# Optimization experiments

Measured on AMD Instinct MI355X. Metric: run time of the kernel, lower is better.

Reference implementation:

```python
import jax, jax.numpy as jnp
import numpy as np

NUM_HEADS = 8
ALPHA = 4.0
BN_EPS = 1e-5


def _dwconv(x, w, pad):
    # x: [B, C, H, W], w: [C, 1, kh, kw] depthwise (groups == C)
    return jax.lax.conv_general_dilated(
        x, w, window_strides=(1, 1), padding=[(pad, pad), (pad, pad)],
        dimension_numbers=('NCHW', 'OIHW', 'NCHW'),
        feature_group_count=x.shape[1])


def _forward(x, qg_w, kv_w, proj_w, proj_b, dwc_w, dwc_b, power_p, scale_p,
             enh_w, bn_gamma, bn_beta, enhance_weight, pos_enc):
    B, N, C = x.shape
    H = W = int(round(N ** 0.5))
    h = NUM_HEADS
    d = C // h

    # qg linear (no bias): [B, N, 2C] -> q, g
    qg = jnp.einsum('bnc,oc->bno', x, qg_w)
    q, g = qg[..., :C], qg[..., C:]

    # SpatialFilterEnhancer on q: depthwise 3x3 conv + BN(train) + ReLU
    qi = q.transpose(0, 2, 1).reshape(B, C, H, W)
    qe = _dwconv(qi, enh_w, pad=1)
    m = qe.mean(axis=(0, 2, 3), keepdims=True)
    var = qe.var(axis=(0, 2, 3), keepdims=True)
    qe = (qe - m) * jax.lax.rsqrt(var + BN_EPS)
    qe = qe * bn_gamma[None, :, None, None] + bn_beta[None, :, None, None]
    qe = jax.nn.relu(qe)
    q_enh = qe.reshape(B, C, N).transpose(0, 2, 1)
    q = q + enhance_weight * q_enh

    # kv linear (sr_ratio == 1 path)
    kv = jnp.einsum('bnc,oc->bno', x, kv_w)
    k, v = kv[..., :C], kv[..., C:]
    k = k + pos_enc  # learned positional encoding, shape [1, N, C]
    n = k.shape[1]

    scale = jax.nn.softplus(scale_p)              # [1, 1, C]
    power = 1.0 + ALPHA * jax.nn.sigmoid(power_p)  # [1, h, 1, d]
    q = q / scale
    k = k / scale

    # split heads: [B, h, N, d]
    q = q.reshape(B, N, h, d).transpose(0, 2, 1, 3)
    k = k.reshape(B, n, h, d).transpose(0, 2, 1, 3)
    v = v.reshape(B, n, h, d).transpose(0, 2, 1, 3)

    # power-law kernel feature maps
    q_pos = jax.nn.relu(q) ** power
    q_neg = jax.nn.relu(-q) ** power
    k_pos = jax.nn.relu(k) ** power
    k_neg = jax.nn.relu(-k) ** power
    q_sim = jnp.concatenate([q_pos, q_neg], axis=-1)   # [B, h, N, 2d]
    q_opp = jnp.concatenate([q_neg, q_pos], axis=-1)
    kf = jnp.concatenate([k_pos, k_neg], axis=-1)      # [B, h, n, 2d]
    v1, v2 = jnp.split(v, 2, axis=-1)                  # [B, h, n, d/2] each

    k_mean = kf.mean(axis=-2)  # [B, h, 2d]
    inv_n = 1.0 / n

    # sim branch
    z = 1.0 / (jnp.einsum('bhnd,bhd->bhn', q_sim, k_mean)[..., None] + 1e-6)
    kv1 = jnp.einsum('bhnd,bhne->bhde', kf, v1) * inv_n  # (n^-0.5)*(n^-0.5)
    x_sim = jnp.einsum('bhnd,bhde->bhne', q_sim, kv1) * z

    # opp branch
    z2 = 1.0 / (jnp.einsum('bhnd,bhd->bhn', q_opp, k_mean)[..., None] + 1e-6)
    kv2 = jnp.einsum('bhnd,bhne->bhde', kf, v2) * inv_n
    x_opp = jnp.einsum('bhnd,bhde->bhne', q_opp, kv2) * z2

    xa = jnp.concatenate([x_sim, x_opp], axis=-1)       # [B, h, N, d]
    xa = xa.transpose(0, 2, 1, 3).reshape(B, N, C)

    # depthwise conv positional branch on v (sr_ratio == 1 -> no interpolate)
    vimg = v.reshape(B * h, H, W, d).transpose(0, 3, 1, 2)  # [B*h, d, H, W]
    vd = _dwconv(vimg, dwc_w, pad=2) + dwc_b[None, :, None, None]
    v_out = vd.reshape(B, C, N).transpose(0, 2, 1)          # [B, N, C]

    out = (xa + v_out) * g
    out = jnp.einsum('bnc,oc->bno', out, proj_w) + proj_b
    return out


def setup_inputs() -> dict:
    key = jax.random.key(0)
    ks = jax.random.split(key, 10)
    B, N, C = 8, 3136, 512
    h = NUM_HEADS
    d = C // h
    f = lambda k, shape, s=0.02: jax.random.normal(k, shape, jnp.float32) * s
    return dict(
        x=jax.random.normal(ks[0], (B, N, C), jnp.float32),
        qg_w=f(ks[1], (2 * C, C)),
        kv_w=f(ks[2], (2 * C, C)),
        proj_w=f(ks[3], (C, C)),
        proj_b=jnp.zeros((C,), jnp.float32),
        dwc_w=f(ks[4], (d, 1, 5, 5), 0.1),
        dwc_b=jnp.zeros((d,), jnp.float32),
        power_p=f(ks[5], (1, h, 1, d), 0.1),
        scale_p=f(ks[6], (1, 1, C), 0.1),
        enh_w=f(ks[7], (C, 1, 3, 3), 0.1),
        bn_gamma=jnp.ones((C,), jnp.float32),
        bn_beta=jnp.zeros((C,), jnp.float32),
        enhance_weight=jnp.float32(0.5),
        pos_enc=f(ks[8], (1, N, C)),
    )


def reference(x, qg_w, kv_w, proj_w, proj_b, dwc_w, dwc_b, power_p, scale_p,
              enh_w, bn_gamma, bn_beta, enhance_weight, pos_enc):
    return _forward(x, qg_w, kv_w, proj_w, proj_b, dwc_w, dwc_b, power_p,
                    scale_p, enh_w, bn_gamma, bn_beta, enhance_weight, pos_enc)
```

## Files before the change

### kernel.cpp

```cpp
#include <hip/hip_runtime.h>
#include <hip/hip_bf16.h>
#include <math.h>

#define CDIM 512
#define NTOK 3136
#define BATCH 8
#define MTOT (BATCH*NTOK)
#define NHEAD 8
#define DHEAD 64
#define HW 56

typedef __attribute__((ext_vector_type(8))) short short8;
typedef __attribute__((ext_vector_type(4))) float f32x4;

__device__ __forceinline__ ushort f2bf(float f) {
    union { float f; unsigned int u; } v; v.f = f;
    unsigned int u = v.u + 0x7FFFu + ((v.u >> 16) & 1u);
    return (ushort)(u >> 16);
}
__device__ __forceinline__ float bf2f(ushort u) {
    union { unsigned int u; float f; } v; v.u = ((unsigned int)u) << 16;
    return v.f;
}

__device__ __forceinline__ void gload_lds16(const void* g, void* lds) {
    __builtin_amdgcn_global_load_lds((const __attribute__((address_space(1))) void*)g,
                                     (__attribute__((address_space(3))) void*)lds,
                                     16, 0, 0);
}

__global__ void prep_kernel(const float* __restrict__ scale_p,
                            const float* __restrict__ power_p,
                            float* __restrict__ inv_scale,
                            float* __restrict__ power) {
    int c = threadIdx.x;
    if (c < CDIM) {
        float s = log1pf(expf(scale_p[c]));
        inv_scale[c] = 1.0f / s;
        power[c] = 1.0f + 4.0f / (1.0f + expf(-power_p[c]));
    }
}

__global__ __launch_bounds__(256) void cvt_bf16_kernel(const float* __restrict__ src,
                                                       ushort* __restrict__ dst, int n4) {
    int i = blockIdx.x * 256 + threadIdx.x;
    if (i < n4) {
        float4 f = ((const float4*)src)[i];
        ushort4 o;
        o.x = f2bf(f.x); o.y = f2bf(f.y); o.z = f2bf(f.z); o.w = f2bf(f.w);
        ((ushort4*)dst)[i] = o;
    }
}

template<int EPI>
__global__ __launch_bounds__(256) void mgemm(const ushort* __restrict__ A,
                                             const ushort* __restrict__ B,
                                             void* __restrict__ out0v,
                                             void* __restrict__ out1v,
                                             const float* __restrict__ aux0,
                                             const float* __restrict__ aux1,
                                             const float* __restrict__ aux2) {
    __shared__ ushort At[128 * 64];
    __shared__ ushort Bt[128 * 64];
    const int t = threadIdx.x;
    const int w = t >> 6, l = t & 63;
    const int m0 = blockIdx.x * 128, o0 = blockIdx.y * 128;
    const int wr = w >> 1, wc = w & 1;
    f32x4 acc[4][4] = {};
    const int r8 = l >> 3, sl = l & 7;
    const int ss = sl ^ r8;

    for (int ks = 0; ks < 8; ++ks) {
        const int k0 = ks * 64;
        #pragma unroll
        for (int c = 0; c < 4; ++c) {
            int rc = (w * 4 + c) * 8 + r8;
            gload_lds16(A + (size_t)(m0 + rc) * CDIM + k0 + ss * 8, At + (w * 4 + c) * 512);
            gload_lds16(B + (size_t)(o0 + rc) * CDIM + k0 + ss * 8, Bt + (w * 4 + c) * 512);
        }
        __syncthreads();
        #pragma unroll
        for (int kk = 0; kk < 2; ++kk) {
            short8 af[4], bfr[4];
            const int sbase = kk * 4 + (l >> 4);
            #pragma unroll
            for (int i = 0; i < 4; ++i) {
                int row = wr * 64 + i * 16 + (l & 15);
                af[i] = *(const short8*)&At[row * 64 + ((sbase ^ (row & 7)) * 8)];
                int rowb = wc * 64 + i * 16 + (l & 15);
                bfr[i] = *(const short8*)&Bt[rowb * 64 + ((sbase ^ (rowb & 7)) * 8)];
            }
            #pragma unroll
            for (int i = 0; i < 4; ++i)
                #pragma unroll
                for (int j = 0; j < 4; ++j)
                    acc[i][j] = __builtin_amdgcn_mfma_f32_16x16x32_bf16(af[i], bfr[j], acc[i][j], 0, 0, 0);
        }
        __syncthreads();
    }
    #pragma unroll
    for (int i = 0; i < 4; ++i) {
        #pragma unroll
        for (int rr = 0; rr < 4; ++rr) {
            int m = m0 + wr * 64 + i * 16 + (l >> 4) * 4 + rr;
            size_t mrow = (size_t)m * CDIM;
            #pragma unroll
            for (int j = 0; j < 4; ++j) {
                int o = o0 + wc * 64 + j * 16 + (l & 15);
                float v = acc[i][j][rr];
                if (EPI == 0) {
                    if (o < CDIM) ((float*)out0v)[mrow + o] = v;
                    else          ((float*)out1v)[mrow + o - CDIM] = v;
                } else if (EPI == 1) {
                    if (o < CDIM) {
                        int n = m % NTOK;
                        float kx = (v + aux0[(size_t)n * CDIM + o]) * aux1[o];
                        float tp = __powf(fabsf(kx), aux2[o]);
                        ushort kfp = kx > 0.f ? f2bf(tp) : (ushort)0;
                        ushort kfn = kx < 0.f ? f2bf(tp) : (ushort)0;
                        ushort* dst = (ushort*)out0v + ((size_t)m * 8 + (o >> 6)) * 128 + (o & 63);
                        dst[0] = kfp;
                        dst[64] = kfn;
                    } else {
                        ((ushort*)out1v)[mrow + o - CDIM] = f2bf(v);
                    }
                } else {
                    ((float*)out0v)[mrow + o] = v + aux0[o];
                }
            }
        }
    }
}

__global__ __launch_bounds__(256) void conv3s_kernel(const float* __restrict__ Q,
                                                     const float* __restrict__ enh_w,
                                                     float* __restrict__ QE,
                                                     float* __restrict__ ssum,
                                                     float* __restrict__ ssq) {
    const int t = threadIdx.x;
    const int c0 = t * 2;
    const int xpos = blockIdx.x;
    const int byc = blockIdx.y;
    const int b = byc >> 2, yc = byc & 3;
    const int y0 = yc * 14;

    float wgt[9][2];
    #pragma unroll
    for (int tap = 0; tap < 9; ++tap) {
        wgt[tap][0] = enh_w[c0 * 9 + tap];
        wgt[tap][1] = enh_w[(c0 + 1) * 9 + tap];
    }
    const size_t base = (size_t)b * NTOK * CDIM + c0;

    float2 win[3][3];
    auto ldrow = [&](int yy, float2* dst) {
        #pragma unroll
        for (int dx = 0; dx < 3; ++dx) {
            int xx = xpos + dx - 1;
            bool ok = (yy >= 0 && yy < HW && xx >= 0 && xx < HW);
            dst[dx] = ok ? *(const float2*)(Q + base + ((size_t)(yy * HW + xx) << 9))
                         : make_float2(0.f, 0.f);
        }
    };
    ldrow(y0 - 1, win[0]);
    ldrow(y0,     win[1]);

    float s1a = 0.f, s2a = 0.f, s1b = 0.f, s2b = 0.f;
    #pragma unroll
    for (int i = 0; i < 14; ++i) {
        int y = y0 + i;
        ldrow(y + 1, win[(i + 2) % 3]);
        float a0 = 0.f, a1 = 0.f;
        #pragma unroll
        for (int dy = 0; dy < 3; ++dy) {
            float2* row = win[(i + dy) % 3];
            #pragma unroll
            for (int dx = 0; dx < 3; ++dx) {
                a0 = fmaf(row[dx].x, wgt[dy * 3 + dx][0], a0);
                a1 = fmaf(row[dx].y, wgt[dy * 3 + dx][1], a1);
            }
        }
        *(float2*)(QE + base + ((size_t)(y * HW + xpos) << 9)) = make_float2(a0, a1);
        s1a += a0; s2a += a0 * a0;
        s1b += a1; s2b += a1 * a1;
    }
    atomicAdd(&ssum[c0], s1a);     atomicAdd(&ssq[c0], s2a);
    atomicAdd(&ssum[c0 + 1], s1b); atomicAdd(&ssq[c0 + 1], s2b);
}

__global__ void bnprep_kernel(const float* __restrict__ ssum, const float* __restrict__ ssq,
                              const float* __restrict__ bn_g, const float* __restrict__ bn_b,
                              float* __restrict__ achan, float* __restrict__ bchan) {
    int c = threadIdx.x;
    if (c < CDIM) {
        const float invM = 1.0f / (float)MTOT;
        float mean = ssum[c] * invM;
        float var  = ssq[c] * invM - mean * mean;
        float a = bn_g[c] * rsqrtf(var + 1e-5f);
        achan[c] = a;
        bchan[c] = bn_b[c] - mean * a;
    }
}

__global__ __launch_bounds__(256) void qfin_kernel(float* __restrict__ Q,
                                                   const float* __restrict__ QE,
                                                   const float* __restrict__ achan,
                                                   const float* __restrict__ bchan,
                                                   const float* __restrict__ inv_scale,
                                                   const float* __restrict__ ewp) {
    int gid = blockIdx.x * 256 + threadIdx.x;
    int c = gid & (CDIM - 1);
    float ew = ewp[0];
    float e = fmaxf(fmaf(achan[c], QE[gid], bchan[c]), 0.f);
    Q[gid] = fmaf(ew, e, Q[gid]) * inv_scale[c];
}

__global__ __launch_bounds__(256) void kvred4_kernel(const ushort* __restrict__ KF,
                                                     const ushort* __restrict__ Vbf,
                                                     float* __restrict__ PKV) {
    const int bh = blockIdx.x, chunk = blockIdx.y;
    const int b = bh >> 3, head = bh & 7;
    const int t = threadIdx.x;
    const int w = t >> 6, l = t & 63;
    const int lr = l & 15;
    const int ns = (l >> 4) * 8;

    const int nbase = b * NTOK + chunk * 224;
    const ushort* kf0 = KF  + ((size_t)(nbase + ns)) * 1024 + head * 128 + (w * 32 + lr);
    const ushort* vb0 = Vbf + ((size_t)(nbase + ns)) * 512  + head * 64  + lr;

    short8 ones;
    #pragma unroll
    for (int j = 0; j < 8; ++j) ones[j] = (lr == 0) ? (short)0x3F80 : (short)0;

    f32x4 acc[2][5] = {};
    for (int tile = 0; tile < 7; ++tile) {
        union { uint u[4]; short8 s; } ua[2], ub[4];
        #pragma unroll
        for (int i = 0; i < 2; ++i) {
            #pragma unroll
            for (int j = 0; j < 4; ++j) {
                uint lo = kf0[i * 16 + (size_t)(2 * j) * 1024];
                uint hi = kf0[i * 16 + (size_t)(2 * j + 1) * 1024];
                ua[i].u[j] = lo | (hi << 16);
            }
        }
        #pragma unroll
        for (int j5 = 0; j5 < 4; ++j5) {
            #pragma unroll
            for (int j = 0; j < 4; ++j) {
                uint lo = vb0[j5 * 16 + (size_t)(2 * j) * 512];
                uint hi = vb0[j5 * 16 + (size_t)(2 * j + 1) * 512];
                ub[j5].u[j] = lo | (hi << 16);
            }
        }
        #pragma unroll
        for (int i = 0; i < 2; ++i) {
            #pragma unroll
            for (int j5 = 0; j5 < 4; ++j5)
                acc[i][j5] = __builtin_amdgcn_mfma_f32_16x16x32_bf16(ua[i].s, ub[j5].s, acc[i][j5], 0, 0, 0);
            acc[i][4] = __builtin_amdgcn_mfma_f32_16x16x32_bf16(ua[i].s, ones, acc[i][4], 0, 0, 0);
        }
        kf0 += (size_t)32 * 1024;
        vb0 += (size_t)32 * 512;
    }
    size_t base = ((size_t)(chunk * 64 + bh)) * 8320;
    #pragma unroll
    for (int i = 0; i < 2; ++i) {
        int d0 = w * 32 + i * 16 + (l >> 4) * 4;
        #pragma unroll
        for (int j = 0; j < 5; ++j) {
            int e = j * 16 + lr;
            if (j < 4 || e == 64)
                *(f32x4*)(PKV + base + (size_t)e * 128 + d0) = acc[i][j];
        }
    }
}

__global__ __launch_bounds__(256) void kvreduce_kernel(const float* __restrict__ PKV,
                                                       float* __restrict__ kvT,
                                                       float* __restrict__ kmean) {
    int gid = blockIdx.x * 256 + threadIdx.x;
    const float inv_n = 1.0f / (float)NTOK;
    float s = 0.f;
    #pragma unroll
    for (int c = 0; c < 14; ++c) s += PKV[(size_t)c * 532480 + gid];
    s *= inv_n;
    int bh = gid / 8320;
    int r  = gid - bh * 8320;
    int e = r >> 7, d = r & 127;
    if (e < 64) kvT[(size_t)bh * 8192 + e * 128 + d] = s;
    else        kmean[bh * 128 + d] = s;
}

__global__ __launch_bounds__(256) void attn_mfma_kernel(const float* __restrict__ Q,
                                                        const float* __restrict__ kvT,
                                                        const float* __restrict__ kmean,
                                                        const float* __restrict__ power,
                                                        float* __restrict__ ATT) {
    __shared__ ushort QF[64 * 128];
    __shared__ ushort BT[80 * 128];
    const int bh = blockIdx.x, tb = blockIdx.y;
    const int b = bh >> 3, head = bh & 7;
    const int t = threadIdx.x;
    const int w = t >> 6, l = t & 63;

    const int c = l;
    const float p = power[head * 64 + c];
    #pragma unroll
    for (int i = 0; i < 16; ++i) {
        int tok = i * 4 + w;
        float q = Q[((size_t)(b * NTOK + tb * 64 + tok)) * CDIM + head * 64 + c];
        float ax = fabsf(q);
        float tp = ax > 0.f ? __powf(ax, p) : 0.f;
        float qp = q > 0.f ? tp : 0.f;
        float qn = q < 0.f ? tp : 0.f;
        int sw = tok & 7;
        QF[tok * 128 + (((c >> 3) ^ sw) * 8) + (c & 7)]       = f2bf(qp);
        QF[tok * 128 + ((((c >> 3) + 8) ^ sw) * 8) + (c & 7)] = f2bf(qn);
    }
    #pragma unroll
    for (int i = 0; i < 5; ++i) {
        int qc = i * 256 + t;
        int row = qc >> 4, s = qc & 15;
        int ls = s ^ (row & 7);
        int d0 = ls * 8;
        short8 ov;
        if (row < 64) {
            int dsel = (row >= 32) ? (d0 ^ 64) : d0;
            const float* src = kvT + (size_t)bh * 8192 + row * 128 + dsel;
            #pragma unroll
            for (int e = 0; e < 8; ++e) ov[e] = (short)f2bf(src[e]);
        } else if (row == 64) {
            const float* src = kmean + bh * 128 + d0;
            #pragma unroll
            for (int e = 0; e < 8; ++e) ov[e] = (short)f2bf(src[e]);
        } else if (row == 65) {
            const float* src = kmean + bh * 128 + (d0 ^ 64);
            #pragma unroll
            for (int e = 0; e < 8; ++e) ov[e] = (short)f2bf(src[e]);
        } else {
            #pragma unroll
            for (int e = 0; e < 8; ++e) ov[e] = 0;
        }
        *(short8*)&BT[row * 128 + s * 8] = ov;
    }
    __syncthreads();

    f32x4 acc[5] = {};
    #pragma unroll
    for (int kk = 0; kk < 4; ++kk) {
        int sbase = kk * 4 + (l >> 4);
        int rowa = w * 16 + (l & 15);
        short8 af = *(const short8*)&QF[rowa * 128 + ((sbase ^ (rowa & 7)) * 8)];
        #pragma unroll
        for (int j = 0; j < 5; ++j) {
            int rowb = j * 16 + (l & 15);
            short8 bf = *(const short8*)&BT[rowb * 128 + ((sbase ^ (rowb & 7)) * 8)];
            acc[j] = __builtin_amdgcn_mfma_f32_16x16x32_bf16(af, bf, acc[j], 0, 0, 0);
        }
    }
    #pragma unroll
    for (int rr = 0; rr < 4; ++rr) {
        float ssim = __shfl(acc[4][rr], (l & 48));
        float sopp = __shfl(acc[4][rr], (l & 48) + 1);
        float zs = 1.f / (ssim + 1e-6f);
        float zo = 1.f / (sopp + 1e-6f);
        int tok = tb * 64 + w * 16 + (l >> 4) * 4 + rr;
        size_t base = ((size_t)(b * NTOK + tok)) * CDIM + head * 64;
        #pragma unroll
        for (int j = 0; j < 4; ++j) {
            int e = j * 16 + (l & 15);
            ATT[base + e] = acc[j][rr] * (j < 2 ? zs : zo);
        }
    }
}

__global__ __launch_bounds__(256) void voutg2_kernel(const ushort* __restrict__ Vbf,
                                                     const float* __restrict__ ATT,
                                                     const float* __restrict__ G,
                                                     const float* __restrict__ dwc_w,
                                                     const float* __restrict__ dwc_b,
                                                     ushort* __restrict__ PRE) {
    const int t = threadIdx.x;
    const int c0 = t * 2;
    const int xpos = blockIdx.x;
    const int byc = blockIdx.y;
    const int b = byc >> 2, yc = byc & 3;
    const int y0 = yc * 14;
    const int dch = c0 & 63;

    float wgt[25][2];
    #pragma unroll
    for (int tap = 0; tap < 25; ++tap) {
        wgt[tap][0] = dwc_w[dch * 25 + tap];
        wgt[tap][1] = dwc_w[(dch + 1) * 25 + tap];
    }
    const float bias0 = dwc_b[dch], bias1 = dwc_b[dch + 1];
    const size_t base = (size_t)b * NTOK * CDIM + c0;

    float2 win[5][5];
    auto ldrow = [&](int yy, float2* dst) {
        #pragma unroll
        for (int dx = 0; dx < 5; ++dx) {
            int xx = xpos + dx - 2;
            bool ok = (yy >= 0 && yy < HW && xx >= 0 && xx < HW);
            if (ok) {
                ushort2 uv = *(const ushort2*)(Vbf + base + ((size_t)(yy * HW + xx) << 9));
                dst[dx] = make_float2(bf2f(uv.x), bf2f(uv.y));
            } else {
                dst[dx] = make_float2(0.f, 0.f);
            }
        }
    };
    ldrow(y0 - 2, win[0]);
    ldrow(y0 - 1, win[1]);
    ldrow(y0,     win[2]);
    ldrow(y0 + 1, win[3]);

    #pragma unroll
    for (int i = 0; i < 14; ++i) {
        int y = y0 + i;
        ldrow(y + 2, win[(i + 4) % 5]);
        float a0 = bias0, a1 = bias1;
        #pragma unroll
        for (int dy = 0; dy < 5; ++dy) {
            float2* row = win[(i + dy) % 5];
            #pragma unroll
            for (int dx = 0; dx < 5; ++dx) {
                a0 = fmaf(row[dx].x, wgt[dy * 5 + dx][0], a0);
                a1 = fmaf(row[dx].y, wgt[dy * 5 + dx][1], a1);
            }
        }
        size_t oidx = base + ((size_t)(y * HW + xpos) << 9);
        float2 att = *(const float2*)(ATT + oidx);
        float2 g   = *(const float2*)(G + oidx);
        ushort2 o;
        o.x = f2bf((att.x + a0) * g.x);
        o.y = f2bf((att.y + a1) * g.y);
        *(ushort2*)(PRE + oidx) = o;
    }
}

extern "C" void kernel_launch(void* const* d_in, const int* in_sizes, int n_in,
                              void* d_out, int out_size, void* d_ws, size_t ws_size,
                              hipStream_t stream) {
    const float* x      = (const float*)d_in[0];
    const float* qg_w   = (const float*)d_in[1];
    const float* kv_w   = (const float*)d_in[2];
    const float* proj_w = (const float*)d_in[3];
    const float* proj_b = (const float*)d_in[4];
    const float* dwc_w  = (const float*)d_in[5];
    const float* dwc_b  = (const float*)d_in[6];
    const float* power_p= (const float*)d_in[7];
    const float* scale_p= (const float*)d_in[8];
    const float* enh_w  = (const float*)d_in[9];
    const float* bn_g   = (const float*)d_in[10];
    const float* bn_b   = (const float*)d_in[11];
    const float* ew_p   = (const float*)d_in[12];
    const float* pos    = (const float*)d_in[13];

    const size_t NELEM = (size_t)MTOT * CDIM;
    float* ws    = (float*)d_ws;
    float* Qb    = ws;
    float* Gb    = ws + NELEM;
    float* Kb    = ws + 2 * NELEM;
    float* Vb    = ws + 3 * NELEM;
    float* QEb   = ws + 4 * NELEM;
    float* SMALL = ws + 5 * NELEM;
    float* ssum  = SMALL;
    float* ssq   = SMALL + 512;
    float* kmean = SMALL + 1024;
    float* kvT   = SMALL + 9216;
    float* invs  = SMALL + 533504;
    float* powr  = SMALL + 534016;
    float* achan = SMALL + 534528;
    float* bchan = SMALL + 535040;
    ushort* Wqg  = (ushort*)(SMALL + 535552);
    ushort* Wkv  = (ushort*)(SMALL + 797696);
    ushort* Wproj= (ushort*)(SMALL + 1059840);

    ushort* Xbf  = (ushort*)QEb;
    ushort* KFbf = (ushort*)Kb;
    ushort* Vbf  = (ushort*)Vb;
    float* PKV   = QEb;
    float* ATTb  = QEb;
    ushort* PREbf= (ushort*)Kb;

    hipMemsetAsync(SMALL, 0, (size_t)1024 * sizeof(float), stream);

    prep_kernel<<<1, 512, 0, stream>>>(scale_p, power_p, invs, powr);

    cvt_bf16_kernel<<<12544, 256, 0, stream>>>(x, Xbf, 3211264);
    cvt_bf16_kernel<<<512, 256, 0, stream>>>(qg_w, Wqg, 131072);
    cvt_bf16_kernel<<<512, 256, 0, stream>>>(kv_w, Wkv, 131072);
    cvt_bf16_kernel<<<256, 256, 0, stream>>>(proj_w, Wproj, 65536);

    dim3 ggrid(196, 8);
    mgemm<0><<<ggrid, 256, 0, stream>>>(Xbf, Wqg, Qb, Gb, nullptr, nullptr, nullptr);
    mgemm<1><<<ggrid, 256, 0, stream>>>(Xbf, Wkv, KFbf, Vbf, pos, invs, powr);

    dim3 cgrid(56, 32);
    conv3s_kernel<<<cgrid, 256, 0, stream>>>(Qb, enh_w, QEb, ssum, ssq);
    bnprep_kernel<<<1, 512, 0, stream>>>(ssum, ssq, bn_g, bn_b, achan, bchan);
    qfin_kernel<<<50176, 256, 0, stream>>>(Qb, QEb, achan, bchan, invs, ew_p);

    kvred4_kernel<<<dim3(64, 14), 256, 0, stream>>>(KFbf, Vbf, PKV);
    kvreduce_kernel<<<2080, 256, 0, stream>>>(PKV, kvT, kmean);

    attn_mfma_kernel<<<dim3(64, 49), 256, 0, stream>>>(Qb, kvT, kmean, powr, ATTb);

    voutg2_kernel<<<cgrid, 256, 0, stream>>>(Vbf, ATTb, Gb, dwc_w, dwc_b, PREbf);

    dim3 pgrid(196, 4);
    mgemm<2><<<pgrid, 256, 0, stream>>>(PREbf, Wproj, (float*)d_out, nullptr, proj_b, nullptr, nullptr);
}
```

Before: 558.2 us.

## Merge qg/kv GEMMs, double-buffer LDS, and remap blocks for XCD locality

Merges the qg and kv projection GEMMs into a single launch over 16 output column tiles, so each X row tile is read by neighbouring blocks while it is still in cache. Both GEMMs now double-buffer the LDS tiles, prefetching the next k-slice while MFMAs run on the current one. A block-index remap spreads tiles round-robin across the 8 XCDs so blocks sharing an X tile land on the same XCD. Double buffering doubles LDS use to 64KB per block, which may cut occupancy.

```diff
diff --git a/kernel.cpp b/kernel.cpp
--- a/kernel.cpp
+++ b/kernel.cpp
@@ -52,33 +52,47 @@
     }
 }
 
-template<int EPI>
-__global__ __launch_bounds__(256) void mgemm(const ushort* __restrict__ A,
-                                             const ushort* __restrict__ B,
-                                             void* __restrict__ out0v,
-                                             void* __restrict__ out1v,
-                                             const float* __restrict__ aux0,
-                                             const float* __restrict__ aux1,
-                                             const float* __restrict__ aux2) {
-    __shared__ ushort At[128 * 64];
-    __shared__ ushort Bt[128 * 64];
+__global__ __launch_bounds__(256) void mgemm_qgkv(const ushort* __restrict__ A,
+                                                  const ushort* __restrict__ Wqg,
+                                                  const ushort* __restrict__ Wkv,
+                                                  float* __restrict__ Qout,
+                                                  float* __restrict__ Gout,
+                                                  ushort* __restrict__ KFout,
+                                                  ushort* __restrict__ Vout,
+                                                  const float* __restrict__ pos,
+                                                  const float* __restrict__ invs,
+                                                  const float* __restrict__ powr) {
+    __shared__ ushort At[2][128 * 64];
+    __shared__ ushort Bt[2][128 * 64];
     const int t = threadIdx.x;
     const int w = t >> 6, l = t & 63;
-    const int m0 = blockIdx.x * 128, o0 = blockIdx.y * 128;
     const int wr = w >> 1, wc = w & 1;
-    f32x4 acc[4][4] = {};
     const int r8 = l >> 3, sl = l & 7;
     const int ss = sl ^ r8;
 
-    for (int ks = 0; ks < 8; ++ks) {
+    const int bid = blockIdx.x;
+    const int idp = (bid & 7) * 392 + (bid >> 3);
+    const int mb = idp >> 4, ob = idp & 15;
+    const int m0 = mb * 128;
+    const ushort* Bp = (ob < 8) ? (Wqg + (size_t)ob * 128 * CDIM)
+                                : (Wkv + (size_t)(ob - 8) * 128 * CDIM);
+
+    auto stage = [&](int buf, int ks) {
         const int k0 = ks * 64;
         #pragma unroll
         for (int c = 0; c < 4; ++c) {
             int rc = (w * 4 + c) * 8 + r8;
-            gload_lds16(A + (size_t)(m0 + rc) * CDIM + k0 + ss * 8, At + (w * 4 + c) * 512);
-            gload_lds16(B + (size_t)(o0 + rc) * CDIM + k0 + ss * 8, Bt + (w * 4 + c) * 512);
-        }
-        __syncthreads();
+            gload_lds16(A + (size_t)(m0 + rc) * CDIM + k0 + ss * 8, &At[buf][(w * 4 + c) * 512]);
+            gload_lds16(Bp + (size_t)rc * CDIM + k0 + ss * 8, &Bt[buf][(w * 4 + c) * 512]);
+        }
+    };
+
+    f32x4 acc[4][4] = {};
+    stage(0, 0);
+    __syncthreads();
+    int cur = 0;
+    for (int ks = 0; ks < 8; ++ks) {
+        if (ks < 7) stage(cur ^ 1, ks + 1);
         #pragma unroll
         for (int kk = 0; kk < 2; ++kk) {
             short8 af[4], bfr[4];
@@ -86,9 +100,9 @@
             #pragma unroll
             for (int i = 0; i < 4; ++i) {
                 int row = wr * 64 + i * 16 + (l & 15);
-                af[i] = *(const short8*)&At[row * 64 + ((sbase ^ (row & 7)) * 8)];
+                af[i] = *(const short8*)&At[cur][row * 64 + ((sbase ^ (row & 7)) * 8)];
                 int rowb = wc * 64 + i * 16 + (l & 15);
-                bfr[i] = *(const short8*)&Bt[rowb * 64 + ((sbase ^ (rowb & 7)) * 8)];
+                bfr[i] = *(const short8*)&Bt[cur][rowb * 64 + ((sbase ^ (rowb & 7)) * 8)];
             }
             #pragma unroll
             for (int i = 0; i < 4; ++i)
@@ -97,7 +111,9 @@
                     acc[i][j] = __builtin_amdgcn_mfma_f32_16x16x32_bf16(af[i], bfr[j], acc[i][j], 0, 0, 0);
         }
         __syncthreads();
-    }
+        cur ^= 1;
+    }
+
     #pragma unroll
     for (int i = 0; i < 4; ++i) {
         #pragma unroll
@@ -106,27 +122,93 @@
             size_t mrow = (size_t)m * CDIM;
             #pragma unroll
             for (int j = 0; j < 4; ++j) {
-                int o = o0 + wc * 64 + j * 16 + (l & 15);
+                int colg = ob * 128 + wc * 64 + j * 16 + (l & 15);
                 float v = acc[i][j][rr];
-                if (EPI == 0) {
-                    if (o < CDIM) ((float*)out0v)[mrow + o] = v;
-                    else          ((float*)out1v)[mrow + o - CDIM] = v;
-                } else if (EPI == 1) {
-                    if (o < CDIM) {
-                        int n = m % NTOK;
-                        float kx = (v + aux0[(size_t)n * CDIM + o]) * aux1[o];
-                        float tp = __powf(fabsf(kx), aux2[o]);
-                        ushort kfp = kx > 0.f ? f2bf(tp) : (ushort)0;
-                        ushort kfn = kx < 0.f ? f2bf(tp) : (ushort)0;
-                        ushort* dst = (ushort*)out0v + ((size_t)m * 8 + (o >> 6)) * 128 + (o & 63);
-                        dst[0] = kfp;
-                        dst[64] = kfn;
-                    } else {
-                        ((ushort*)out1v)[mrow + o - CDIM] = f2bf(v);
-                    }
+                if (colg < 512) {
+                    Qout[mrow + colg] = v;
+                } else if (colg < 1024) {
+                    Gout[mrow + colg - 512] = v;
+                } else if (colg < 1536) {
+                    int oc = colg - 1024;
+                    int n = m % NTOK;
+                    float kx = (v + pos[(size_t)n * CDIM + oc]) * invs[oc];
+                    float tp = __powf(fabsf(kx), powr[oc]);
+                    ushort* dst = KFout + ((size_t)m * 8 + (oc >> 6)) * 128 + (oc & 63);
+                    dst[0]  = kx > 0.f ? f2bf(tp) : (ushort)0;
+                    dst[64] = kx < 0.f ? f2bf(tp) : (ushort)0;
                 } else {
-                    ((float*)out0v)[mrow + o] = v + aux0[o];
+                    Vout[mrow + colg - 1536] = f2bf(v);
                 }
+            }
+        }
+    }
+}
+
+__global__ __launch_bounds__(256) void mgemm_proj(const ushort* __restrict__ A,
+                                                  const ushort* __restrict__ W,
+                                                  float* __restrict__ out,
+                                                  const float* __restrict__ pb) {
+    __shared__ ushort At[2][128 * 64];
+    __shared__ ushort Bt[2][128 * 64];
+    const int t = threadIdx.x;
+    const int w = t >> 6, l = t & 63;
+    const int wr = w >> 1, wc = w & 1;
+    const int r8 = l >> 3, sl = l & 7;
+    const int ss = sl ^ r8;
+
+    const int bid = blockIdx.x;
+    const int idp = (bid & 7) * 98 + (bid >> 3);
+    const int mb = idp >> 2, ob = idp & 3;
+    const int m0 = mb * 128;
+    const ushort* Bp = W + (size_t)ob * 128 * CDIM;
+
+    auto stage = [&](int buf, int ks) {
+        const int k0 = ks * 64;
+        #pragma unroll
+        for (int c = 0; c < 4; ++c) {
+            int rc = (w * 4 + c) * 8 + r8;
+            gload_lds16(A + (size_t)(m0 + rc) * CDIM + k0 + ss * 8, &At[buf][(w * 4 + c) * 512]);
+            gload_lds16(Bp + (size_t)rc * CDIM + k0 + ss * 8, &Bt[buf][(w * 4 + c) * 512]);
+        }
+    };
+
+    f32x4 acc[4][4] = {};
+    stage(0, 0);
+    __syncthreads();
+    int cur = 0;
+    for (int ks = 0; ks < 8; ++ks) {
+        if (ks < 7) stage(cur ^ 1, ks + 1);
+        #pragma unroll
+        for (int kk = 0; kk < 2; ++kk) {
+            short8 af[4], bfr[4];
+            const int sbase = kk * 4 + (l >> 4);
+            #pragma unroll
+            for (int i = 0; i < 4; ++i) {
+                int row = wr * 64 + i * 16 + (l & 15);
+                af[i] = *(const short8*)&At[cur][row * 64 + ((sbase ^ (row & 7)) * 8)];
+                int rowb = wc * 64 + i * 16 + (l & 15);
+                bfr[i] = *(const short8*)&Bt[cur][rowb * 64 + ((sbase ^ (rowb & 7)) * 8)];
+            }
+            #pragma unroll
+            for (int i = 0; i < 4; ++i)
+                #pragma unroll
+                for (int j = 0; j < 4; ++j)
+                    acc[i][j] = __builtin_amdgcn_mfma_f32_16x16x32_bf16(af[i], bfr[j], acc[i][j], 0, 0, 0);
+        }
+        __syncthreads();
+        cur ^= 1;
+    }
+
+    #pragma unroll
+    for (int i = 0; i < 4; ++i) {
+        #pragma unroll
+        for (int rr = 0; rr < 4; ++rr) {
+            int m = m0 + wr * 64 + i * 16 + (l >> 4) * 4 + rr;
+            size_t mrow = (size_t)m * CDIM;
+            #pragma unroll
+            for (int j = 0; j < 4; ++j) {
+                int colg = ob * 128 + wc * 64 + j * 16 + (l & 15);
+                out[mrow + colg] = acc[i][j][rr] + pb[colg];
             }
         }
     }
@@ -496,9 +578,7 @@
     cvt_bf16_kernel<<<512, 256, 0, stream>>>(kv_w, Wkv, 131072);
     cvt_bf16_kernel<<<256, 256, 0, stream>>>(proj_w, Wproj, 65536);
 
-    dim3 ggrid(196, 8);
-    mgemm<0><<<ggrid, 256, 0, stream>>>(Xbf, Wqg, Qb, Gb, nullptr, nullptr, nullptr);
-    mgemm<1><<<ggrid, 256, 0, stream>>>(Xbf, Wkv, KFbf, Vbf, pos, invs, powr);
+    mgemm_qgkv<<<3136, 256, 0, stream>>>(Xbf, Wqg, Wkv, Qb, Gb, KFbf, Vbf, pos, invs, powr);
 
     dim3 cgrid(56, 32);
     conv3s_kernel<<<cgrid, 256, 0, stream>>>(Qb, enh_w, QEb, ssum, ssq);
@@ -512,6 +592,5 @@
 
     voutg2_kernel<<<cgrid, 256, 0, stream>>>(Vbf, ATTb, Gb, dwc_w, dwc_b, PREbf);
 
-    dim3 pgrid(196, 4);
-    mgemm<2><<<pgrid, 256, 0, stream>>>(PREbf, Wproj, (float*)d_out, nullptr, proj_b, nullptr, nullptr);
-}
+    mgemm_proj<<<784, 256, 0, stream>>>(PREbf, Wproj, (float*)d_out, proj_b);
+}
```

Result: slower. 573.1 us (+2.7%).
